# Performance work log

Measured on AMD Instinct MI355X. Metric: run time of the kernel, lower is better.

The kernel has to match this reference:

```python
import jax, jax.numpy as jnp
import numpy as np

EPS = 1e-5


def _bn_silu(x, gamma, beta):
    # train-mode BatchNorm2d (biased batch stats over N,H,W) followed by SiLU
    m = jnp.mean(x, axis=(0, 2, 3), keepdims=True)
    v = jnp.var(x, axis=(0, 2, 3), keepdims=True)
    y = gamma[None, :, None, None] * (x - m) * jax.lax.rsqrt(v + EPS) + beta[None, :, None, None]
    return y * jax.nn.sigmoid(y)


def _deform_conv2d(x, offset, w, b):
    # x: [B,C,H,W]; offset: [B,2*9,H,W] as (dy,dx) pairs per 3x3 tap; w: [Co,C,3,3]
    B, C, H, W = x.shape
    Co = w.shape[0]
    off = offset.reshape(B, 9, 2, H, W)
    k = jnp.arange(9)
    ky = (k // 3 - 1).astype(x.dtype)  # kernel tap offsets, pad=1 so centered
    kx = (k % 3 - 1).astype(x.dtype)
    py = jnp.arange(H, dtype=x.dtype)[None, None, :, None] + ky[None, :, None, None] + off[:, :, 0]
    px = jnp.arange(W, dtype=x.dtype)[None, None, None, :] + kx[None, :, None, None] + off[:, :, 1]
    y0 = jnp.floor(py)
    x0 = jnp.floor(px)
    wy1 = py - y0
    wx1 = px - x0
    xf = x.reshape(B, C, H * W)

    def corner(yi, xi, cw):
        # zero-padded bilinear corner: mask out-of-bounds taps via weight
        valid = (yi >= 0) & (yi < H) & (xi >= 0) & (xi < W)
        idx = jnp.clip(yi, 0, H - 1) * W + jnp.clip(xi, 0, W - 1)
        g = jnp.take_along_axis(xf, idx.reshape(B, 1, -1), axis=2).reshape(B, C, 9, H, W)
        return g * (cw * valid.astype(x.dtype))[:, None]

    y0i = y0.astype(jnp.int32)
    x0i = x0.astype(jnp.int32)
    s = corner(y0i, x0i, (1 - wy1) * (1 - wx1))
    s = s + corner(y0i, x0i + 1, (1 - wy1) * wx1)
    s = s + corner(y0i + 1, x0i, wy1 * (1 - wx1))
    s = s + corner(y0i + 1, x0i + 1, wy1 * wx1)
    out = jnp.einsum('bckhw,ock->bohw', s, w.reshape(Co, C, 9))
    return out + b[None, :, None, None]


def _conv_transpose(x, w, stride, pad):
    # torch ConvTranspose2d: weight layout [Cin, Cout, kh, kw]
    k = w.shape[2]
    wf = jnp.flip(w, (2, 3)).transpose(1, 0, 2, 3)  # -> OIHW, spatially flipped
    p = k - 1 - pad
    return jax.lax.conv_general_dilated(
        x, wf, (1, 1), [(p, p), (p, p)], lhs_dilation=(stride, stride),
        dimension_numbers=('NCHW', 'OIHW', 'NCHW'))


def setup_inputs() -> dict:
    key = jax.random.key(0)
    ks = jax.random.split(key, 4)
    B, C, Co, H, W = 16, 256, 256, 32, 32
    r = lambda k, s, sc: jax.random.normal(k, s, jnp.float32) * sc
    return {
        'x': r(ks[0], (B, C, H, W), 1.0),
        'w_off': r(ks[1], (18, C, 3, 3), 0.01),
        'b_off': jnp.zeros((18,), jnp.float32),
        'w_def': r(ks[2], (Co, C, 3, 3), 0.02),
        'b_def': jnp.zeros((Co,), jnp.float32),
        'gamma1': jnp.ones((Co,), jnp.float32),
        'beta1': jnp.zeros((Co,), jnp.float32),
        'w_dc': r(ks[3], (Co, Co, 4, 4), 0.02),
        'gamma2': jnp.ones((Co,), jnp.float32),
        'beta2': jnp.zeros((Co,), jnp.float32),
    }


def reference(x, w_off, b_off, w_def, b_def, gamma1, beta1, w_dc, gamma2, beta2):
    offset = jax.lax.conv_general_dilated(
        x, w_off, (1, 1), [(1, 1), (1, 1)],
        dimension_numbers=('NCHW', 'OIHW', 'NCHW')) + b_off[None, :, None, None]
    y = _deform_conv2d(x, offset, w_def, b_def)
    y = _bn_silu(y, gamma1, beta1)
    y = _conv_transpose(y, w_dc, 2, 1)
    return _bn_silu(y, gamma2, beta2)
```

## Files before the change

kernel.cpp:

```cpp
#include <hip/hip_runtime.h>
#include <math.h>

#ifdef __has_builtin
#if __has_builtin(__builtin_amdgcn_global_load_lds)
#define HAS_GLL 1
#endif
#endif
#ifndef HAS_GLL
#define HAS_GLL 0
#endif

typedef __attribute__((ext_vector_type(8))) short short8v;
typedef __attribute__((ext_vector_type(4))) float float4v;

__device__ __forceinline__ unsigned short f2bf(float f) {
    unsigned int u = __float_as_uint(f);
    u += 0x7fffu + ((u >> 16) & 1u);
    return (unsigned short)(u >> 16);
}

__device__ __forceinline__ float silu(float y) { return y / (1.f + expf(-y)); }

__device__ __forceinline__ void stage1k(const void* gsrc, void* ldsbase) {
#if HAS_GLL
    __builtin_amdgcn_global_load_lds((const __attribute__((address_space(1))) unsigned int*)gsrc,
                                     (__attribute__((address_space(3))) unsigned int*)ldsbase,
                                     16, 0, 0);
#else
    int lane = threadIdx.x & 63;
    *(float4*)((char*)ldsbase + lane * 16) = *(const float4*)gsrc;
#endif
}

__global__ __launch_bounds__(256) void k_prep_all(const float* __restrict__ w_def,
                                                  const float* __restrict__ w_dc,
                                                  const float* __restrict__ w_off,
                                                  const float* __restrict__ x,
                                                  unsigned short* __restrict__ A1,
                                                  unsigned short* __restrict__ A2,
                                                  unsigned short* __restrict__ A2off,
                                                  unsigned short* __restrict__ xT) {
    int blk = blockIdx.x;
    int t = threadIdx.x;
    __shared__ unsigned short tl[32][36];
    if (blk < 4096) {
        int i = blk * 256 + t;
        int ci = i & 255;
        int tq = (i >> 8) & 3;
        int co = (i >> 10) & 255;
        int p  = i >> 18;
        int ph = p >> 1, pw = p & 1;
        int ty = tq >> 1, tx = tq & 1;
        int kh = 2 * ty + 1 - ph;
        int kw = 2 * tx + 1 - pw;
        A2[i] = f2bf(w_dc[((ci * 256 + co) * 4 + kh) * 4 + kw]);
    } else if (blk < 6400) {
        int i = (blk - 4096) * 256 + t;
        A1[i] = f2bf(w_def[i]);
    } else if (blk < 6688) {
        int i = (blk - 6400) * 256 + t;
        int slot = i & 31;
        int oc = (i >> 5) & 31;
        int rest = i >> 10;
        int tap = rest % 9;
        int cc8 = rest / 9;
        int cgrp = (slot >> 3) ^ ((oc >> 1) & 3);
        int c = cc8 * 32 + (cgrp << 3) + (slot & 7);
        unsigned short v = 0;
        if (oc < 18) v = f2bf(w_off[(size_t)oc * 2304 + c * 9 + tap]);
        A2off[i] = v;
    } else {
        int blk2 = blk - 6688;
        int hw0 = (blk2 & 31) * 32;
        int c0 = ((blk2 >> 5) & 7) * 32;
        int b = blk2 >> 8;
        {
            int c_l = t >> 3, w4 = (t & 7) * 4;
            float4 v = *(const float4*)&x[(size_t)((b * 256 + c0 + c_l) * 1024) + hw0 + w4];
            tl[c_l][w4 + 0] = f2bf(v.x);
            tl[c_l][w4 + 1] = f2bf(v.y);
            tl[c_l][w4 + 2] = f2bf(v.z);
            tl[c_l][w4 + 3] = f2bf(v.w);
        }
        __syncthreads();
        {
            int hw_l = t >> 3, c4 = (t & 7) * 4;
            unsigned int s0 = tl[c4 + 0][hw_l];
            unsigned int s1 = tl[c4 + 1][hw_l];
            unsigned int s2 = tl[c4 + 2][hw_l];
            unsigned int s3 = tl[c4 + 3][hw_l];
            uint2 pk;
            pk.x = s0 | (s1 << 16);
            pk.y = s2 | (s3 << 16);
            *(uint2*)&xT[(size_t)((b * 1024 + hw0 + hw_l) * 256) + c0 + c4] = pk;
        }
    }
}

__global__ __launch_bounds__(256) void k_off_gemm(const unsigned short* __restrict__ A2off,
                                                  const unsigned short* __restrict__ xT,
                                                  const float* __restrict__ b_off,
                                                  float* __restrict__ off) {
    int hp = blockIdx.x, b = blockIdx.y;
    int h0 = hp * 2;
    int t = threadIdx.x;
    int lane = t & 63, wid = t >> 6;
    int l15 = lane & 15, g = lane >> 4;
    int swg = (l15 >> 1) & 3;
    __shared__ __align__(16) unsigned short As[9 * 32 * 32];
    __shared__ __align__(16) unsigned short Bsx[4 * 34 * 32];
    float4v acc[2];
    float4v z = {0.f, 0.f, 0.f, 0.f};
    acc[0] = z; acc[1] = z;

    int pos = wid * 16 + l15;
    int py = pos >> 5, px = pos & 31;

    for (int cc8 = 0; cc8 < 8; ++cc8) {
        __syncthreads();
        for (int idx = t; idx < 1152; idx += 256)
            stage1k(A2off + (size_t)cc8 * 9216 + idx * 8, (char*)As + idx * 16);
        for (int idx = t; idx < 544; idx += 256) {
            int r = idx / 136;
            int rem = idx - r * 136;
            int col = rem >> 2;
            int sgrp = rem & 3;
            int grp = sgrp ^ ((col >> 1) & 3);
            int h = h0 - 1 + r;
            int w = col - 1;
            uint4 v = {0u, 0u, 0u, 0u};
            if (h >= 0 && h < 32 && w >= 0 && w < 32)
                v = *(const uint4*)&xT[(size_t)((b * 1024 + h * 32 + w) * 256) + cc8 * 32 + grp * 8];
            *(uint4*)((char*)Bsx + ((r * 34 + col) << 6) + (sgrp << 4)) = v;
        }
        __syncthreads();
#pragma unroll
        for (int tap = 0; tap < 9; ++tap) {
            int ky = tap / 3, kx = tap - ky * 3;
            int col = px + kx;
            int rowr = py + ky;
            short8v bbf = *(const short8v*)((const char*)Bsx + ((rowr * 34 + col) << 6) +
                                            ((g ^ ((col >> 1) & 3)) << 4));
            short8v a0 = *(const short8v*)((const char*)As + tap * 2048 + l15 * 64 + ((g ^ swg) << 4));
            short8v a1 = *(const short8v*)((const char*)As + tap * 2048 + (16 + l15) * 64 + ((g ^ swg) << 4));
            acc[0] = __builtin_amdgcn_mfma_f32_16x16x32_bf16(a0, bbf, acc[0], 0, 0, 0);
            acc[1] = __builtin_amdgcn_mfma_f32_16x16x32_bf16(a1, bbf, acc[1], 0, 0, 0);
        }
    }
    int h = h0 + py;
#pragma unroll
    for (int r = 0; r < 4; ++r) {
        int oc = g * 4 + r;
        off[((size_t)(b * 18 + oc) << 10) + (h << 5) + px] = acc[0][r] + b_off[oc];
    }
    if (g == 0) {
#pragma unroll
        for (int r = 0; r < 2; ++r) {
            int oc = 16 + r;
            off[((size_t)(b * 18 + oc) << 10) + (h << 5) + px] = acc[1][r] + b_off[oc];
        }
    }
}

__global__ __launch_bounds__(576) void k_sample(const float* __restrict__ x,
                                                const float* __restrict__ off,
                                                unsigned short* __restrict__ S) {
    int cg = blockIdx.x, b = blockIdx.y, half = blockIdx.z;
    int cbase = cg * 8;
    int t = threadIdx.x;
    int k = t >> 6, lane = t & 63;
    __shared__ __align__(16) unsigned int xpl[4 * 1156];
    __shared__ __align__(16) unsigned short sS[72 * 66];

    for (int u = t; u < 1024; u += 576) {
        int p = u >> 8, row = (u >> 3) & 31, cq = (u & 7) << 2;
        const float* src0 = x + ((size_t)(b * 256 + cbase + 2 * p) << 10) + (row << 5) + cq;
        float4 a = *(const float4*)src0;
        float4 c = *(const float4*)(src0 + 1024);
        uint4 pk;
        pk.x = (unsigned int)f2bf(a.x) | ((unsigned int)f2bf(c.x) << 16);
        pk.y = (unsigned int)f2bf(a.y) | ((unsigned int)f2bf(c.y) << 16);
        pk.z = (unsigned int)f2bf(a.z) | ((unsigned int)f2bf(c.z) << 16);
        pk.w = (unsigned int)f2bf(a.w) | ((unsigned int)f2bf(c.w) << 16);
        *(uint4*)&xpl[p * 1156 + row * 36 + cq] = pk;
    }

    int wr_row = t / 9, wr_q = t - wr_row * 9;
    const float* offk0 = off + ((size_t)(b * 18 + 2 * k) << 10);
    const float* offk1 = off + ((size_t)(b * 18 + 2 * k + 1) << 10);
    int ky = k / 3 - 1, kx = k % 3 - 1;
    __syncthreads();

    for (int ci = 0; ci < 8; ++ci) {
        int chunk = half * 8 + ci;
        int pos = chunk * 64 + lane;
        int h = pos >> 5, w = pos & 31;
        float dy = offk0[pos];
        float dx = offk1[pos];
        float py = (float)(h + ky) + dy;
        float px = (float)(w + kx) + dx;
        float fy = floorf(py), fx = floorf(px);
        int y0i = (int)fy, x0i = (int)fx;
        float wy = py - fy, wxf = px - fx;
        float vy0 = (y0i >= 0 && y0i < 32) ? 1.f : 0.f;
        float vy1 = (y0i >= -1 && y0i < 31) ? 1.f : 0.f;
        float vx0 = (x0i >= 0 && x0i < 32) ? 1.f : 0.f;
        float vx1 = (x0i >= -1 && x0i < 31) ? 1.f : 0.f;
        int y0c = min(max(y0i, 0), 31), y1c = min(max(y0i + 1, 0), 31);
        int x0c = min(max(x0i, 0), 31), x1c = min(max(x0i + 1, 0), 31);
        float w00 = (1.f - wy) * (1.f - wxf) * vy0 * vx0;
        float w01 = (1.f - wy) * wxf * vy0 * vx1;
        float w10 = wy * (1.f - wxf) * vy1 * vx0;
        float w11 = wy * wxf * vy1 * vx1;
        int a00 = y0c * 36 + x0c, a01 = y0c * 36 + x1c;
        int a10 = y1c * 36 + x0c, a11 = y1c * 36 + x1c;
#pragma unroll
        for (int p = 0; p < 4; ++p) {
            const unsigned int* pl = xpl + p * 1156;
            unsigned int c00 = pl[a00], c01 = pl[a01], c10 = pl[a10], c11 = pl[a11];
            float e00 = __uint_as_float(c00 << 16), o00 = __uint_as_float(c00 & 0xFFFF0000u);
            float e01 = __uint_as_float(c01 << 16), o01 = __uint_as_float(c01 & 0xFFFF0000u);
            float e10 = __uint_as_float(c10 << 16), o10 = __uint_as_float(c10 & 0xFFFF0000u);
            float e11 = __uint_as_float(c11 << 16), o11 = __uint_as_float(c11 & 0xFFFF0000u);
            float ve = w00 * e00 + w01 * e01 + w10 * e10 + w11 * e11;
            float vo = w00 * o00 + w01 * o01 + w10 * o10 + w11 * o11;
            sS[((2 * p) * 9 + k) * 66 + lane] = f2bf(ve);
            sS[((2 * p + 1) * 9 + k) * 66 + lane] = f2bf(vo);
        }
        __syncthreads();
        {
            int basekc = wr_q * 8;
            unsigned int s0 = sS[(basekc + 0) * 66 + wr_row];
            unsigned int s1 = sS[(basekc + 1) * 66 + wr_row];
            unsigned int s2 = sS[(basekc + 2) * 66 + wr_row];
            unsigned int s3 = sS[(basekc + 3) * 66 + wr_row];
            unsigned int s4 = sS[(basekc + 4) * 66 + wr_row];
            unsigned int s5 = sS[(basekc + 5) * 66 + wr_row];
            unsigned int s6 = sS[(basekc + 6) * 66 + wr_row];
            unsigned int s7 = sS[(basekc + 7) * 66 + wr_row];
            uint4 qv;
            qv.x = s0 | (s1 << 16);
            qv.y = s2 | (s3 << 16);
            qv.z = s4 | (s5 << 16);
            qv.w = s6 | (s7 << 16);
            *(uint4*)(S + (size_t)(b * 1024 + chunk * 64 + wr_row) * 2304 + cg * 72 + wr_q * 8) = qv;
        }
        __syncthreads();
    }
}

__global__ __launch_bounds__(256) void k_gemm1(const unsigned short* __restrict__ A1,
                                               const unsigned short* __restrict__ S,
                                               const float* __restrict__ b_def,
                                               unsigned short* __restrict__ y1b,
                                               float* __restrict__ pstats1) {
    int nb = blockIdx.x, mb = blockIdx.y;
    int t = threadIdx.x;
    int lane = t & 63, wid = t >> 6;
    int wm = wid >> 1, wn = wid & 1;
    int l15 = lane & 15, g = lane >> 4;
    __shared__ __align__(16) unsigned short As[2][8192];
    __shared__ __align__(16) unsigned short Bs[2][4096];
    int m0 = mb * 128, n0 = nb * 64;
    int b = n0 >> 10, pos0 = n0 & 1023;

    const unsigned short* srcA[4];
    int dA[4];
    const unsigned short* srcB[2];
    int dB[2];
#pragma unroll
    for (int it = 0; it < 4; ++it) {
        int idx = t + it * 256;
        int r = idx >> 3, s8 = idx & 7, c = s8 ^ (r & 7);
        srcA[it] = A1 + (size_t)(m0 + r) * 2304 + c * 8;
        dA[it] = idx * 8;
    }
#pragma unroll
    for (int it = 0; it < 2; ++it) {
        int idx = t + it * 256;
        int r = idx >> 3, s8 = idx & 7, c = s8 ^ (r & 7);
        srcB[it] = S + (size_t)(n0 + r) * 2304 + c * 8;
        dB[it] = idx * 8;
    }

    float4v acc[4][2];
    float4v z = {0.f, 0.f, 0.f, 0.f};
#pragma unroll
    for (int i = 0; i < 4; ++i) { acc[i][0] = z; acc[i][1] = z; }

#pragma unroll
    for (int it = 0; it < 4; ++it) stage1k(srcA[it], &As[0][dA[it]]);
#pragma unroll
    for (int it = 0; it < 2; ++it) stage1k(srcB[it], &Bs[0][dB[it]]);
    __syncthreads();

    for (int step = 0; step < 36; ++step) {
        int cur = step & 1;
        if (step < 35) {
            int koff = (step + 1) * 64;
#pragma unroll
            for (int it = 0; it < 4; ++it) stage1k(srcA[it] + koff, &As[cur ^ 1][dA[it]]);
#pragma unroll
            for (int it = 0; it < 2; ++it) stage1k(srcB[it] + koff, &Bs[cur ^ 1][dB[it]]);
        }
        __builtin_amdgcn_s_setprio(1);
#pragma unroll
        for (int kk = 0; kk < 2; ++kk) {
            short8v a[4], bb[2];
#pragma unroll
            for (int mi = 0; mi < 4; ++mi) {
                int row = wm * 64 + mi * 16 + l15;
                int slot = ((kk << 2) + g) ^ (row & 7);
                a[mi] = *(const short8v*)((const char*)&As[cur][0] + row * 128 + slot * 16);
            }
#pragma unroll
            for (int ni = 0; ni < 2; ++ni) {
                int row = wn * 32 + ni * 16 + l15;
                int slot = ((kk << 2) + g) ^ (row & 7);
                bb[ni] = *(const short8v*)((const char*)&Bs[cur][0] + row * 128 + slot * 16);
            }
#pragma unroll
            for (int mi = 0; mi < 4; ++mi)
#pragma unroll
                for (int ni = 0; ni < 2; ++ni)
                    acc[mi][ni] = __builtin_amdgcn_mfma_f32_16x16x32_bf16(a[mi], bb[ni], acc[mi][ni], 0, 0, 0);
        }
        __builtin_amdgcn_s_setprio(0);
        __syncthreads();
    }

    float* sred  = (float*)&As[0][0];
    float* s2red = sred + 256;
#pragma unroll
    for (int mi = 0; mi < 4; ++mi) {
#pragma unroll
        for (int r = 0; r < 4; ++r) {
            int co = m0 + wm * 64 + mi * 16 + g * 4 + r;
            float bv = b_def[co];
            unsigned short* dst = y1b + ((size_t)(b * 256 + co) << 10) + pos0;
            float s = 0.f, s2 = 0.f;
#pragma unroll
            for (int ni = 0; ni < 2; ++ni) {
                float v = acc[mi][ni][r] + bv;
                dst[wn * 32 + ni * 16 + l15] = f2bf(v);
                s += v;
                s2 += v * v;
            }
#pragma unroll
            for (int m = 8; m >= 1; m >>= 1) {
                s  += __shfl_xor(s, m, 64);
                s2 += __shfl_xor(s2, m, 64);
            }
            if (l15 == 0) {
                int col = wm * 64 + mi * 16 + g * 4 + r;
                sred[col * 2 + wn]  = s;
                s2red[col * 2 + wn] = s2;
            }
        }
    }
    __syncthreads();
    if (t < 128) {
        float s  = sred[t * 2] + sred[t * 2 + 1];
        float s2 = s2red[t * 2] + s2red[t * 2 + 1];
        int ch = m0 + t;
        pstats1[ch * 256 + nb] = s;
        pstats1[65536 + ch * 256 + nb] = s2;
    }
}

__global__ __launch_bounds__(256) void k_gemm2(const unsigned short* __restrict__ A2,
                                               const unsigned short* __restrict__ y1T,
                                               unsigned short* __restrict__ outP,
                                               float* __restrict__ pstats2) {
    int nb = blockIdx.x, mb = blockIdx.y, p = blockIdx.z;
    int ph = p >> 1, pw = p & 1;
    int t = threadIdx.x;
    int lane = t & 63, wid = t >> 6;
    int wm = wid >> 1, wn = wid & 1;
    int l15 = lane & 15, g = lane >> 4;
    __shared__ __align__(16) unsigned short As[2][8192];
    __shared__ __align__(16) unsigned short Bs[2][8192];
    int m0 = mb * 128, n0 = nb * 128;
    int b = n0 >> 10, pos0 = n0 & 1023, oh0 = pos0 >> 5;

    int dtab[4];
#pragma unroll
    for (int tap = 0; tap < 4; ++tap) {
        int ty = tap >> 1, tx = tap & 1;
        int dy = ph ? (1 - ty) : (-ty);
        int dx = pw ? (1 - tx) : (-tx);
        dtab[tap] = (dy * 34 + dx) * 256;
    }
    const unsigned short* srcA[4];
    const unsigned short* srcB[4];
    int dstoff[4];
#pragma unroll
    for (int it = 0; it < 4; ++it) {
        int idx = t + it * 256;
        int r = idx >> 3, s8 = idx & 7, c = s8 ^ (r & 7);
        srcA[it] = A2 + (size_t)(p * 256 + m0 + r) * 1024 + c * 8;
        int ih = oh0 + (r >> 5) + 1;
        int iw = (r & 31) + 1;
        srcB[it] = y1T + ((size_t)(b * 34 + ih) * 34 + iw) * 256 + c * 8;
        dstoff[it] = idx * 8;
    }

    float4v acc[4][4];
    float4v z = {0.f, 0.f, 0.f, 0.f};
#pragma unroll
    for (int i = 0; i < 4; ++i)
#pragma unroll
        for (int j = 0; j < 4; ++j) acc[i][j] = z;

#pragma unroll
    for (int it = 0; it < 4; ++it) {
        stage1k(srcA[it], &As[0][dstoff[it]]);
        stage1k(srcB[it] + dtab[0], &Bs[0][dstoff[it]]);
    }
    __syncthreads();

#pragma unroll
    for (int step = 0; step < 16; ++step) {
        int cur = step & 1;
        if (step < 15) {
            int ns = step + 1;
            int tap = ns >> 2;
            int koff = ns * 64;
            int boff = dtab[tap] + (ns & 3) * 64;
#pragma unroll
            for (int it = 0; it < 4; ++it) {
                stage1k(srcA[it] + koff, &As[cur ^ 1][dstoff[it]]);
                stage1k(srcB[it] + boff, &Bs[cur ^ 1][dstoff[it]]);
            }
        }
        __builtin_amdgcn_s_setprio(1);
#pragma unroll
        for (int kk = 0; kk < 2; ++kk) {
            short8v a[4], bb[4];
#pragma unroll
            for (int mi = 0; mi < 4; ++mi) {
                int row = wm * 64 + mi * 16 + l15;
                int slot = ((kk << 2) + g) ^ (row & 7);
                a[mi] = *(const short8v*)((const char*)&As[cur][0] + row * 128 + slot * 16);
            }
#pragma unroll
            for (int ni = 0; ni < 4; ++ni) {
                int row = wn * 64 + ni * 16 + l15;
                int slot = ((kk << 2) + g) ^ (row & 7);
                bb[ni] = *(const short8v*)((const char*)&Bs[cur][0] + row * 128 + slot * 16);
            }
#pragma unroll
            for (int mi = 0; mi < 4; ++mi)
#pragma unroll
                for (int ni = 0; ni < 4; ++ni)
                    acc[mi][ni] = __builtin_amdgcn_mfma_f32_16x16x32_bf16(a[mi], bb[ni], acc[mi][ni], 0, 0, 0);
        }
        __builtin_amdgcn_s_setprio(0);
        __syncthreads();
    }
#pragma unroll
    for (int mi = 0; mi < 4; ++mi) {
#pragma unroll
        for (int r = 0; r < 4; ++r) {
            int co = m0 + wm * 64 + mi * 16 + g * 4 + r;
            unsigned short* dst = outP + ((size_t)((p * 16 + b) * 256 + co) << 10) + pos0;
#pragma unroll
            for (int ni = 0; ni < 4; ++ni)
                dst[wn * 64 + ni * 16 + l15] = f2bf(acc[mi][ni][r]);
        }
    }
    float* sred  = (float*)&As[0][0];
    float* s2red = sred + 256;
#pragma unroll
    for (int mi = 0; mi < 4; ++mi) {
#pragma unroll
        for (int r = 0; r < 4; ++r) {
            float s = 0.f, s2 = 0.f;
#pragma unroll
            for (int ni = 0; ni < 4; ++ni) {
                float v = acc[mi][ni][r];
                s += v;
                s2 += v * v;
            }
#pragma unroll
            for (int m = 8; m >= 1; m >>= 1) {
                s  += __shfl_xor(s, m, 64);
                s2 += __shfl_xor(s2, m, 64);
            }
            if (l15 == 0) {
                int col = wm * 64 + mi * 16 + g * 4 + r;
                sred[col * 2 + wn]  = s;
                s2red[col * 2 + wn] = s2;
            }
        }
    }
    __syncthreads();
    if (t < 128) {
        float s  = sred[t * 2] + sred[t * 2 + 1];
        float s2 = s2red[t * 2] + s2red[t * 2 + 1];
        int row = p * 128 + nb;
        int ch = m0 + t;
        pstats2[ch * 512 + row] = s;
        pstats2[131072 + ch * 512 + row] = s2;
    }
}

__global__ __launch_bounds__(256) void k_bnfin_par(const float* __restrict__ pstats, int nparts,
                                                   float n,
                                                   float* __restrict__ mean, float* __restrict__ rstd) {
    int ch = blockIdx.x;
    int t = threadIdx.x;
    float s = 0.f, s2 = 0.f;
    for (int j = t; j < nparts; j += 256) {
        s  += pstats[ch * nparts + j];
        s2 += pstats[256 * nparts + ch * nparts + j];
    }
    __shared__ float rs[256], rs2[256];
    rs[t] = s; rs2[t] = s2;
    __syncthreads();
    for (int d = 128; d > 0; d >>= 1) {
        if (t < d) { rs[t] += rs[t + d]; rs2[t] += rs2[t + d]; }
        __syncthreads();
    }
    if (t == 0) {
        float m = rs[0] / n;
        float var = rs2[0] / n - m * m;
        mean[ch] = m;
        rstd[ch] = rsqrtf(var + 1e-5f);
    }
}

__global__ __launch_bounds__(256) void k_bnsilu_padT(const unsigned short* __restrict__ y1b,
                                                     const float* __restrict__ mean,
                                                     const float* __restrict__ rstd,
                                                     const float* __restrict__ gamma,
                                                     const float* __restrict__ beta,
                                                     unsigned short* __restrict__ y1T) {
    int py = blockIdx.x, cg = blockIdx.y, b = blockIdx.z;
    int c0 = cg * 32;
    int t = threadIdx.x;
    uint2 zz; zz.x = 0u; zz.y = 0u;
    if (py == 0 || py == 33) {
        for (int u = t; u < 272; u += 256) {
            int col = u >> 3, c4 = (u & 7) * 4;
            *(uint2*)&y1T[((size_t)(b * 34 + py) * 34 + col) * 256 + c0 + c4] = zz;
        }
        return;
    }
    __shared__ unsigned short tl[32][36];
    int iy = py - 1;
    {
        int c_l = t >> 3, px4 = (t & 7) * 4;
        int ch = c0 + c_l;
        float m = mean[ch], rs = rstd[ch], ga = gamma[ch], be = beta[ch];
        uint2 v = *(const uint2*)&y1b[(size_t)((b * 256 + ch) << 10) + (iy << 5) + px4];
        float f0 = __uint_as_float(v.x << 16), f1 = __uint_as_float(v.x & 0xFFFF0000u);
        float f2 = __uint_as_float(v.y << 16), f3 = __uint_as_float(v.y & 0xFFFF0000u);
        tl[c_l][px4 + 0] = f2bf(silu(ga * (f0 - m) * rs + be));
        tl[c_l][px4 + 1] = f2bf(silu(ga * (f1 - m) * rs + be));
        tl[c_l][px4 + 2] = f2bf(silu(ga * (f2 - m) * rs + be));
        tl[c_l][px4 + 3] = f2bf(silu(ga * (f3 - m) * rs + be));
    }
    __syncthreads();
    {
        int px = t >> 3, c4 = (t & 7) * 4;
        unsigned int s0 = tl[c4 + 0][px];
        unsigned int s1 = tl[c4 + 1][px];
        unsigned int s2 = tl[c4 + 2][px];
        unsigned int s3 = tl[c4 + 3][px];
        uint2 pk;
        pk.x = s0 | (s1 << 16);
        pk.y = s2 | (s3 << 16);
        *(uint2*)&y1T[((size_t)(b * 34 + py) * 34 + (px + 1)) * 256 + c0 + c4] = pk;
    }
    if (t < 16) {
        int col = (t >> 3) ? 33 : 0;
        int c4 = (t & 7) * 4;
        *(uint2*)&y1T[((size_t)(b * 34 + py) * 34 + col) * 256 + c0 + c4] = zz;
    }
}

__global__ __launch_bounds__(256) void k_bnsilu_out(const unsigned short* __restrict__ outP,
                                                    const float* __restrict__ mean,
                                                    const float* __restrict__ rstd,
                                                    const float* __restrict__ gamma,
                                                    const float* __restrict__ beta,
                                                    float* __restrict__ out) {
    unsigned int i = blockIdx.x * 256 + threadIdx.x;
    int ow4 = i & 15;
    int oh = (i >> 4) & 63;
    int co = (i >> 10) & 255;
    int b  = i >> 18;
    int p0 = (oh & 1) * 2;
    int pos = ((oh >> 1) << 5) + ow4 * 2;
    const unsigned short* pl0 = outP + ((size_t)((p0 * 16 + b) * 256 + co) << 10) + pos;
    const unsigned short* pl1 = pl0 + ((size_t)16 * 256 << 10);
    unsigned int ue = *(const unsigned int*)pl0;
    unsigned int uo = *(const unsigned int*)pl1;
    float ex = __uint_as_float(ue << 16), ey = __uint_as_float(ue & 0xFFFF0000u);
    float ox = __uint_as_float(uo << 16), oy = __uint_as_float(uo & 0xFFFF0000u);
    float m = mean[co], rs = rstd[co], ga = gamma[co], be = beta[co];
    float4 v;
    v.x = silu(ga * (ex - m) * rs + be);
    v.y = silu(ga * (ox - m) * rs + be);
    v.z = silu(ga * (ey - m) * rs + be);
    v.w = silu(ga * (oy - m) * rs + be);
    *(float4*)&out[((size_t)(b * 256 + co) << 12) + (oh << 6) + ow4 * 4] = v;
}

extern "C" void kernel_launch(void* const* d_in, const int* in_sizes, int n_in,
                              void* d_out, int out_size, void* d_ws, size_t ws_size,
                              hipStream_t stream) {
    const float* x      = (const float*)d_in[0];
    const float* w_off  = (const float*)d_in[1];
    const float* b_off  = (const float*)d_in[2];
    const float* w_def  = (const float*)d_in[3];
    const float* b_def  = (const float*)d_in[4];
    const float* gamma1 = (const float*)d_in[5];
    const float* beta1  = (const float*)d_in[6];
    const float* w_dc   = (const float*)d_in[7];
    const float* gamma2 = (const float*)d_in[8];
    const float* beta2  = (const float*)d_in[9];
    float* out = (float*)d_out;

    char* base = (char*)d_ws;
    unsigned short* S    = (unsigned short*)base;
    unsigned short* y1b  = (unsigned short*)(base + 75497472);
    unsigned short* y1T  = (unsigned short*)(base + 92274688);
    unsigned short* A1   = (unsigned short*)(base + 101744640);
    unsigned short* A2   = (unsigned short*)(base + 102924288);
    float*          off  = (float*)(base + 105021440);
    float*          stats = (float*)(base + 106201088);
    float* mean1 = stats, *rstd1 = stats + 256, *mean2 = stats + 512, *rstd2 = stats + 768;
    float* pstats1 = off;
    float* pstats2 = off;
    unsigned short* xT    = (unsigned short*)base;
    unsigned short* A2off = (unsigned short*)(base + 8388608);
    unsigned short* outP = (unsigned short*)base;

    k_prep_all<<<10784, 256, 0, stream>>>(w_def, w_dc, w_off, x, A1, A2, A2off, xT);
    k_off_gemm<<<dim3(16, 16), 256, 0, stream>>>(A2off, xT, b_off, off);
    k_sample<<<dim3(32, 16, 2), 576, 0, stream>>>(x, off, S);
    k_gemm1<<<dim3(256, 2), 256, 0, stream>>>(A1, S, b_def, y1b, pstats1);
    k_bnfin_par<<<256, 256, 0, stream>>>(pstats1, 256, 16384.f, mean1, rstd1);
    k_bnsilu_padT<<<dim3(34, 8, 16), 256, 0, stream>>>(y1b, mean1, rstd1, gamma1, beta1, y1T);
    k_gemm2<<<dim3(128, 2, 4), 256, 0, stream>>>(A2, y1T, outP, pstats2);
    k_bnfin_par<<<256, 256, 0, stream>>>(pstats2, 512, 65536.f, mean2, rstd2);
    k_bnsilu_out<<<16384, 256, 0, stream>>>(outP, mean2, rstd2, gamma2, beta2, out);
}
```

Baseline: 184.7 us.

## Use partial vmcnt waits and raw barriers to overlap prefetch with MFMA

Both GEMM main loops now issue the next K-tile's global-to-LDS loads first, then wait only for the previous tile's loads (vmcnt(6)/vmcnt(8)) before a raw s_barrier, instead of the __syncthreads which drains all outstanding memory ops. The goal is to keep the next stage's loads in flight while the current stage's MFMAs run. The last step is peeled out, and the buffer index becomes a compile-time constant through a macro. This relies on vmcnt counting matching the number of stage1k loads exactly. If the compiler inserts other vector-memory ops, the wait could be wrong and cause a data race.

```diff
diff --git a/kernel.cpp b/kernel.cpp
--- a/kernel.cpp
+++ b/kernel.cpp
@@ -292,42 +292,54 @@
     for (int it = 0; it < 4; ++it) stage1k(srcA[it], &As[0][dA[it]]);
 #pragma unroll
     for (int it = 0; it < 2; ++it) stage1k(srcB[it], &Bs[0][dB[it]]);
-    __syncthreads();
-
-    for (int step = 0; step < 36; ++step) {
+
+#define G1_COMPUTE(CUR)                                                                     \
+    {                                                                                       \
+        __builtin_amdgcn_s_setprio(1);                                                      \
+        _Pragma("unroll")                                                                   \
+        for (int kk = 0; kk < 2; ++kk) {                                                    \
+            short8v a[4], bb[2];                                                            \
+            _Pragma("unroll")                                                               \
+            for (int mi = 0; mi < 4; ++mi) {                                                \
+                int row = wm * 64 + mi * 16 + l15;                                          \
+                int slot = ((kk << 2) + g) ^ (row & 7);                                     \
+                a[mi] = *(const short8v*)((const char*)&As[CUR][0] + row * 128 + slot * 16);\
+            }                                                                               \
+            _Pragma("unroll")                                                               \
+            for (int ni = 0; ni < 2; ++ni) {                                                \
+                int row = wn * 32 + ni * 16 + l15;                                          \
+                int slot = ((kk << 2) + g) ^ (row & 7);                                     \
+                bb[ni] = *(const short8v*)((const char*)&Bs[CUR][0] + row * 128 + slot * 16);\
+            }                                                                               \
+            _Pragma("unroll")                                                               \
+            for (int mi = 0; mi < 4; ++mi)                                                  \
+                _Pragma("unroll")                                                           \
+                for (int ni = 0; ni < 2; ++ni)                                              \
+                    acc[mi][ni] = __builtin_amdgcn_mfma_f32_16x16x32_bf16(a[mi], bb[ni],    \
+                                                                          acc[mi][ni], 0, 0, 0);\
+        }                                                                                   \
+        __builtin_amdgcn_s_setprio(0);                                                      \
+    }
+
+    for (int step = 0; step < 35; ++step) {
         int cur = step & 1;
-        if (step < 35) {
-            int koff = (step + 1) * 64;
-#pragma unroll
-            for (int it = 0; it < 4; ++it) stage1k(srcA[it] + koff, &As[cur ^ 1][dA[it]]);
-#pragma unroll
-            for (int it = 0; it < 2; ++it) stage1k(srcB[it] + koff, &Bs[cur ^ 1][dB[it]]);
-        }
-        __builtin_amdgcn_s_setprio(1);
-#pragma unroll
-        for (int kk = 0; kk < 2; ++kk) {
-            short8v a[4], bb[2];
-#pragma unroll
-            for (int mi = 0; mi < 4; ++mi) {
-                int row = wm * 64 + mi * 16 + l15;
-                int slot = ((kk << 2) + g) ^ (row & 7);
-                a[mi] = *(const short8v*)((const char*)&As[cur][0] + row * 128 + slot * 16);
-            }
-#pragma unroll
-            for (int ni = 0; ni < 2; ++ni) {
-                int row = wn * 32 + ni * 16 + l15;
-                int slot = ((kk << 2) + g) ^ (row & 7);
-                bb[ni] = *(const short8v*)((const char*)&Bs[cur][0] + row * 128 + slot * 16);
-            }
-#pragma unroll
-            for (int mi = 0; mi < 4; ++mi)
-#pragma unroll
-                for (int ni = 0; ni < 2; ++ni)
-                    acc[mi][ni] = __builtin_amdgcn_mfma_f32_16x16x32_bf16(a[mi], bb[ni], acc[mi][ni], 0, 0, 0);
-        }
-        __builtin_amdgcn_s_setprio(0);
-        __syncthreads();
-    }
+        int koff = (step + 1) * 64;
+#pragma unroll
+        for (int it = 0; it < 4; ++it) stage1k(srcA[it] + koff, &As[cur ^ 1][dA[it]]);
+#pragma unroll
+        for (int it = 0; it < 2; ++it) stage1k(srcB[it] + koff, &Bs[cur ^ 1][dB[it]]);
+        asm volatile("s_waitcnt vmcnt(6)" ::: "memory");
+        __builtin_amdgcn_s_barrier();
+        asm volatile("" ::: "memory");
+        if (cur == 0) { G1_COMPUTE(0); } else { G1_COMPUTE(1); }
+        asm volatile("" ::: "memory");
+        __builtin_amdgcn_s_barrier();
+    }
+    asm volatile("s_waitcnt vmcnt(0)" ::: "memory");
+    __builtin_amdgcn_s_barrier();
+    asm volatile("" ::: "memory");
+    G1_COMPUTE(1)
+#undef G1_COMPUTE
 
     float* sred  = (float*)&As[0][0];
     float* s2red = sred + 256;
@@ -417,47 +429,60 @@
         stage1k(srcA[it], &As[0][dstoff[it]]);
         stage1k(srcB[it] + dtab[0], &Bs[0][dstoff[it]]);
     }
-    __syncthreads();
-
-#pragma unroll
-    for (int step = 0; step < 16; ++step) {
+
+#define G2_COMPUTE(CUR)                                                                     \
+    {                                                                                       \
+        __builtin_amdgcn_s_setprio(1);                                                      \
+        _Pragma("unroll")                                                                   \
+        for (int kk = 0; kk < 2; ++kk) {                                                    \
+            short8v a[4], bb[4];                                                            \
+            _Pragma("unroll")                                                               \
+            for (int mi = 0; mi < 4; ++mi) {                                                \
+                int row = wm * 64 + mi * 16 + l15;                                          \
+                int slot = ((kk << 2) + g) ^ (row & 7);                                     \
+                a[mi] = *(const short8v*)((const char*)&As[CUR][0] + row * 128 + slot * 16);\
+            }                                                                               \
+            _Pragma("unroll")                                                               \
+            for (int ni = 0; ni < 4; ++ni) {                                                \
+                int row = wn * 64 + ni * 16 + l15;                                          \
+                int slot = ((kk << 2) + g) ^ (row & 7);                                     \
+                bb[ni] = *(const short8v*)((const char*)&Bs[CUR][0] + row * 128 + slot * 16);\
+            }                                                                               \
+            _Pragma("unroll")                                                               \
+            for (int mi = 0; mi < 4; ++mi)                                                  \
+                _Pragma("unroll")                                                           \
+                for (int ni = 0; ni < 4; ++ni)                                              \
+                    acc[mi][ni] = __builtin_amdgcn_mfma_f32_16x16x32_bf16(a[mi], bb[ni],    \
+                                                                          acc[mi][ni], 0, 0, 0);\
+        }                                                                                   \
+        __builtin_amdgcn_s_setprio(0);                                                      \
+    }
+
+#pragma unroll
+    for (int step = 0; step < 15; ++step) {
         int cur = step & 1;
-        if (step < 15) {
-            int ns = step + 1;
-            int tap = ns >> 2;
-            int koff = ns * 64;
-            int boff = dtab[tap] + (ns & 3) * 64;
-#pragma unroll
-            for (int it = 0; it < 4; ++it) {
-                stage1k(srcA[it] + koff, &As[cur ^ 1][dstoff[it]]);
-                stage1k(srcB[it] + boff, &Bs[cur ^ 1][dstoff[it]]);
-            }
-        }
-        __builtin_amdgcn_s_setprio(1);
-#pragma unroll
-        for (int kk = 0; kk < 2; ++kk) {
-            short8v a[4], bb[4];
-#pragma unroll
-            for (int mi = 0; mi < 4; ++mi) {
-                int row = wm * 64 + mi * 16 + l15;
-                int slot = ((kk << 2) + g) ^ (row & 7);
-                a[mi] = *(const short8v*)((const char*)&As[cur][0] + row * 128 + slot * 16);
-            }
-#pragma unroll
-            for (int ni = 0; ni < 4; ++ni) {
-                int row = wn * 64 + ni * 16 + l15;
-                int slot = ((kk << 2) + g) ^ (row & 7);
-                bb[ni] = *(const short8v*)((const char*)&Bs[cur][0] + row * 128 + slot * 16);
-            }
-#pragma unroll
-            for (int mi = 0; mi < 4; ++mi)
-#pragma unroll
-                for (int ni = 0; ni < 4; ++ni)
-                    acc[mi][ni] = __builtin_amdgcn_mfma_f32_16x16x32_bf16(a[mi], bb[ni], acc[mi][ni], 0, 0, 0);
-        }
-        __builtin_amdgcn_s_setprio(0);
-        __syncthreads();
-    }
+        int ns = step + 1;
+        int tap = ns >> 2;
+        int koff = ns * 64;
+        int boff = dtab[tap] + (ns & 3) * 64;
+#pragma unroll
+        for (int it = 0; it < 4; ++it) {
+            stage1k(srcA[it] + koff, &As[cur ^ 1][dstoff[it]]);
+            stage1k(srcB[it] + boff, &Bs[cur ^ 1][dstoff[it]]);
+        }
+        asm volatile("s_waitcnt vmcnt(8)" ::: "memory");
+        __builtin_amdgcn_s_barrier();
+        asm volatile("" ::: "memory");
+        if (cur == 0) { G2_COMPUTE(0); } else { G2_COMPUTE(1); }
+        asm volatile("" ::: "memory");
+        __builtin_amdgcn_s_barrier();
+    }
+    asm volatile("s_waitcnt vmcnt(0)" ::: "memory");
+    __builtin_amdgcn_s_barrier();
+    asm volatile("" ::: "memory");
+    G2_COMPUTE(1)
+#undef G2_COMPUTE
+
 #pragma unroll
     for (int mi = 0; mi < 4; ++mi) {
 #pragma unroll
```

Result: no change. 184.0 us (-0.3%).
